# Kernel optimization log

Hardware: AMD Instinct MI355X
Metric: run time of the kernel (lower is better)

Reference implementation:

```python
import jax, jax.numpy as jnp
import numpy as np

IMAGE_SIZE = 288.0
LAMBDA_NOOBJ = 0.5
LAMBDA_COOR = 5.0
_ANCHOR_DIMS = np.array([[0.24, 0.24], [0.12, 0.12], [0.08, 0.08], [0.28, 0.28], [0.15, 0.15]], np.float32)
ANCHORS = jnp.concatenate([jnp.full((5, 2), 0.5, jnp.float32), jnp.asarray(_ANCHOR_DIMS)], axis=1)  # [cx,cy,w,h]


def _corners(box):
    # matches torch _format_bbox column order used in _get_iou: (x1, x2, y1, y2)
    cx, cy, w, h = box[..., 0], box[..., 1], box[..., 2], box[..., 3]
    return cx - w / 2, cx + w / 2, cy - h / 2, cy + h / 2


def _iou(b1, b2):
    x1a, x2a, y1a, y2a = _corners(b1)
    x1b, x2b, y1b, y2b = _corners(b2)
    iw = jnp.minimum(x2a, x2b) - jnp.maximum(x1a, x1b) + 1.0
    ih = jnp.minimum(y2a, y2b) - jnp.maximum(y1a, y1b) + 1.0
    inter = iw * ih
    a1 = (x2a - x1a + 1.0) * (y2a - y1a + 1.0)
    a2 = (x2b - x1b + 1.0) * (y2b - y1b + 1.0)
    return inter / (a1 + a2 - inter + 1e-16)


def setup_inputs() -> dict:
    key = jax.random.key(0)
    k1, k2, k3, k4 = jax.random.split(key, 4)
    B, G, A, T = 32, 36, 5, 8
    return {
        "bbox_prediction": jax.random.normal(k1, (B, G, G, A, 5), jnp.float32),
        "landmarks_prediction": jax.random.normal(k2, (B, G, G, A, 68, 2), jnp.float32),
        "bbox_target": jax.random.uniform(k3, (B, T, 4), jnp.float32),
        "landmarks_target": jax.random.uniform(k4, (B, T, 68, 2), jnp.float32),
    }


def _forward(bbox_prediction, landmarks_prediction, bbox_target, landmarks_target):
    B, G, _, A, _ = bbox_prediction.shape
    T = bbox_target.shape[1]
    N = B * G * G * A

    valid = bbox_target.sum(-1) != 0  # (B,T)
    gx = bbox_target[..., 0] * G
    gy = bbox_target[..., 1] * G
    gi = jnp.floor(gx).astype(jnp.int32)  # int(gt_x)
    gj = jnp.floor(gy).astype(jnp.int32)
    fx = gx - gi
    fy = gy - gj
    gt_anchor_box = jnp.stack([fx, fy, bbox_target[..., 2], bbox_target[..., 3]], -1)  # (B,T,4)

    # vectorized anchor assignment (replaces per-target python loop)
    anchor_iou = _iou(gt_anchor_box[:, :, None, :], ANCHORS[None, None, :, :])  # (B,T,A)
    best_a = jnp.argmax(anchor_iou, -1).astype(jnp.int32)
    log_box = jnp.log1p(gt_anchor_box)  # (B,T,4) -- torch stores log1p form

    lin = ((jnp.arange(B)[:, None] * G + gj) * G + gi) * A + best_a  # (B,T) flat (b,j,i,a)
    lin = jnp.where(valid, lin, N)  # invalid targets -> dump slot N

    obj = jnp.zeros(N + 1, jnp.float32).at[lin.ravel()].set(1.0)[:N].reshape(B, G, G, A)
    noobj = 1.0 - obj

    t_ids = jnp.broadcast_to(jnp.arange(T, dtype=jnp.int32), (B, T))
    seg_last = jax.ops.segment_max(t_ids.ravel(), lin.ravel(), num_segments=N + 1)
    winner = (seg_last[lin] == t_ids) & valid
    lin_w = jnp.where(winner, lin, N).ravel()

    gt_boxes = jnp.zeros((N + 1, 4), jnp.float32).at[lin_w].set(log_box.reshape(-1, 4))[:N].reshape(B, G, G, A, 4)
    gt_lm = jnp.zeros((N + 1, 136), jnp.float32).at[lin_w].set(landmarks_target.reshape(B * T, 136))[:N].reshape(B, G, G, A, 136)

    nobj = jnp.maximum(obj.sum(), 1.0)

    # NME over object cells (masked-mean expressed as weighted sum -> static shapes)
    diff = landmarks_prediction.reshape(B, G, G, A, 136) - gt_lm
    dist = jnp.sqrt(jnp.sum(diff * diff, -1))  # (B,G,G,A)
    wh = gt_boxes[..., 2] * gt_boxes[..., 3]  # note: log1p(w)*log1p(h), as in torch
    norm = jnp.sqrt(jnp.where(obj > 0, wh, 1.0)) * IMAGE_SIZE * 68.0 * nobj
    nme = jnp.sum(obj * dist / norm)

    # localization: SmoothL1 (beta=1), mean over masked elements
    d = bbox_prediction[..., :4] - gt_boxes
    ad = jnp.abs(d)
    sl1 = jnp.where(ad < 1.0, 0.5 * d * d, ad - 0.5)
    loc_loss = LAMBDA_COOR * jnp.sum(obj[..., None] * sl1) / (nobj * 4.0)

    # confidence: MSE on noobj (target 0) + MSE on obj (target 1)
    conf_pred = bbox_prediction[..., 4]
    n_noobj = jnp.maximum(noobj.sum(), 1.0)
    conf_loss = LAMBDA_NOOBJ * jnp.sum(noobj * conf_pred ** 2) / n_noobj + jnp.sum(obj * (conf_pred - 1.0) ** 2) / nobj

    # best predicted bbox per target (IoU of log1p gt box vs raw cell predictions, as in torch)
    cell_pred = bbox_prediction[jnp.arange(B)[:, None], gj, gi]  # (B,T,A,5)
    pred_iou = _iou(log_box[:, :, None, :], cell_pred[..., :4])  # (B,T,A)
    best_p = jnp.argmax(pred_iou, -1)
    best = jnp.take_along_axis(cell_pred, best_p[..., None, None], axis=2)[:, :, 0]  # (B,T,5)
    x1, x2, y1, y2 = _corners(best[..., :4])
    best_pred = jnp.where(valid[..., None], jnp.stack([x1, x2, y1, y2, best[..., 4]], -1), 0.0)

    return nme, loc_loss, conf_loss, best_pred


def reference(bbox_prediction, landmarks_prediction, bbox_target, landmarks_target):
    return _forward(bbox_prediction, landmarks_prediction, bbox_target, landmarks_target)
```

## Files before the change

kernel.cpp:

```cpp
#include <hip/hip_runtime.h>
#include <math.h>

#define Gc 36
#define Ac 5
#define Bc 32
#define Tc 8
#define NCELLS (Bc*Gc*Gc*Ac)
#define NFLOATS (NCELLS*5)
#define NF4 (NFLOATS/4)
#define NT 256
#define CONF_BLOCKS 128


__device__ __forceinline__ void target_meta(const float* __restrict__ bbox_tgt,
                                            int tid, bool& valid, int& gi, int& gj,
                                            float& fx, float& fy, float& w, float& h,
                                            int& best_a) {
    const int b = tid >> 3, t = tid & 7;
    const float* tg = bbox_tgt + (size_t)(b * Tc + t) * 4;
    float x = tg[0], y = tg[1];
    w = tg[2]; h = tg[3];
    valid = ((x + y + w + h) != 0.0f);
    float gx = x * (float)Gc, gy = y * (float)Gc;
    gi = (int)floorf(gx); gj = (int)floorf(gy);
    fx = gx - floorf(gx); fy = gy - floorf(gy);

    float x1a = fx - w * 0.5f, x2a = fx + w * 0.5f;
    float y1a = fy - h * 0.5f, y2a = fy + h * 0.5f;
    float a1 = (x2a - x1a + 1.0f) * (y2a - y1a + 1.0f);
    const float adim[Ac] = {0.24f, 0.12f, 0.08f, 0.28f, 0.15f};
    best_a = 0;
    float best_iou = -1e30f;
    for (int a = 0; a < Ac; ++a) {
        float x1b = 0.5f - adim[a] * 0.5f, x2b = 0.5f + adim[a] * 0.5f;
        float iw = fminf(x2a, x2b) - fmaxf(x1a, x1b) + 1.0f;
        float ih = fminf(y2a, x2b) - fmaxf(y1a, x1b) + 1.0f;
        float inter = iw * ih;
        float a2 = (x2b - x1b + 1.0f) * (x2b - x1b + 1.0f);
        float iou = inter / (a1 + a2 - inter + 1e-16f);
        if (iou > best_iou) { best_iou = iou; best_a = a; }
    }
}

__global__ __launch_bounds__(NT) void k1_conf_meta(
        const float* __restrict__ bbox_pred,
        const float* __restrict__ bbox_tgt,
        float* __restrict__ ws_f, int* __restrict__ ws_i) {
    if (blockIdx.x < CONF_BLOCKS) {
        __shared__ float red[NT];
        const float4* p4 = (const float4*)bbox_pred;
        float acc = 0.0f;
        for (int j = blockIdx.x * NT + threadIdx.x; j < NF4;
             j += CONF_BLOCKS * NT) {
            float4 f = p4[j];
            int r = (4 * j) % 5;
            float v = (r == 4) ? f.x : (r == 3) ? f.y : (r == 2) ? f.z
                    : (r == 1) ? f.w : 0.0f;
            acc += v * v;
        }
        red[threadIdx.x] = acc;
        __syncthreads();
        for (int s = NT / 2; s > 0; s >>= 1) {
            if (threadIdx.x < s) red[threadIdx.x] += red[threadIdx.x + s];
            __syncthreads();
        }
        if (threadIdx.x == 0) ws_f[blockIdx.x] = red[0];
    } else {
        __shared__ int s_lin[NT];
        const int tid = threadIdx.x;
        const int b = tid >> 3, t = tid & 7;
        bool valid; int gi, gj, best_a; float fx, fy, w, h;
        target_meta(bbox_tgt, tid, valid, gi, gj, fx, fy, w, h, best_a);
        int lin = valid ? (((b * Gc + gj) * Gc + gi) * Ac + best_a) : NCELLS;
        s_lin[tid] = lin;
        __syncthreads();
        bool winner = valid;
        if (valid) {
            for (int t2 = t + 1; t2 < Tc; ++t2)
                if (s_lin[(b << 3) + t2] == lin) { winner = false; break; }
        }
        ws_i[256 + tid] = lin;
        ws_i[512 + tid] = winner ? 1 : 0;
    }
}

__global__ __launch_bounds__(64) void k2_lmdist(
        const float* __restrict__ lm_pred,
        const float* __restrict__ lm_tgt,
        const int* __restrict__ ws_i,
        float* __restrict__ ws_f) {
    const int tgt = blockIdx.x;
    const int lane = threadIdx.x;
    int winner = ws_i[512 + tgt];
    int lin = ws_i[256 + tgt];
    float acc = 0.0f;
    if (winner && lane < 34) {
        const float4* lp = (const float4*)(lm_pred + (size_t)lin * 136);
        const float4* lt = (const float4*)(lm_tgt + (size_t)tgt * 136);
        float4 a = lp[lane], b = lt[lane];
        float dx = a.x - b.x, dy = a.y - b.y, dz = a.z - b.z, dw = a.w - b.w;
        acc = dx * dx + dy * dy + dz * dz + dw * dw;
    }
    for (int off = 32; off > 0; off >>= 1)
        acc += __shfl_down(acc, off, 64);
    if (lane == 0) ws_f[1024 + tgt] = winner ? sqrtf(acc) : 0.0f;
}

__device__ __forceinline__ float block_sum(float v, float* red, int tid) {
    red[tid] = v;
    __syncthreads();
    for (int s = NT / 2; s > 0; s >>= 1) {
        if (tid < s) red[tid] += red[tid + s];
        __syncthreads();
    }
    float r = red[0];
    __syncthreads();
    return r;
}

__global__ __launch_bounds__(NT) void k3_final(
        const float* __restrict__ bbox_pred,
        const float* __restrict__ bbox_tgt,
        const float* __restrict__ ws_f,
        const int* __restrict__ ws_i,
        float* __restrict__ out) {
    const int tid = threadIdx.x;
    const int b = tid >> 3, t = tid & 7;
    __shared__ float s_red[NT];
    __shared__ int s_cnt[NT];

    bool valid; int gi, gj, best_a; float fx, fy, w, h;
    target_meta(bbox_tgt, tid, valid, gi, gj, fx, fy, w, h, best_a);
    int lin = ws_i[256 + tid];
    int winner = ws_i[512 + tid];
    float dist = ws_f[1024 + tid];

    float l0 = log1pf(fx), l1 = log1pf(fy), l2 = log1pf(w), l3 = log1pf(h);

    float c_nme = 0.0f, c_sl1 = 0.0f, c_cobj = 0.0f, c_csq = 0.0f;
    if (winner) {
        const float* bp = bbox_pred + (size_t)lin * 5;
        float conf = bp[4];
        c_cobj = (conf - 1.0f) * (conf - 1.0f);
        c_csq = conf * conf;
        float lb[4] = {l0, l1, l2, l3};
        for (int k = 0; k < 4; ++k) {
            float d = bp[k] - lb[k];
            float ad = fabsf(d);
            c_sl1 += (ad < 1.0f) ? 0.5f * d * d : (ad - 0.5f);
        }
        c_nme = dist / (sqrtf(l2 * l3) * 288.0f * 68.0f);
    }

    s_cnt[tid] = winner;
    __syncthreads();
    for (int s = NT / 2; s > 0; s >>= 1) {
        if (tid < s) s_cnt[tid] += s_cnt[tid + s];
        __syncthreads();
    }
    int cnt = s_cnt[0];
    __syncthreads();
    float nobj = fmaxf((float)cnt, 1.0f);
    float n_noobj = fmaxf((float)(NCELLS - cnt), 1.0f);

    float sum_nme  = block_sum(c_nme, s_red, tid);
    float sum_sl1  = block_sum(c_sl1, s_red, tid);
    float sum_cobj = block_sum(c_cobj, s_red, tid);
    float sum_csq  = block_sum(c_csq, s_red, tid);
    float s_total  = block_sum(tid < CONF_BLOCKS ? ws_f[tid] : 0.0f, s_red, tid);

    if (tid == 0) {
        out[0] = sum_nme / nobj;
        out[1] = 5.0f * sum_sl1 / (nobj * 4.0f);
        out[2] = 0.5f * (s_total - sum_csq) / n_noobj + sum_cobj / nobj;
    }

    const float* cp = bbox_pred + (size_t)((b * Gc + gj) * Gc + gi) * Ac * 5;
    float x1g = l0 - l2 * 0.5f, x2g = l0 + l2 * 0.5f;
    float y1g = l1 - l3 * 0.5f, y2g = l1 + l3 * 0.5f;
    float ag = (x2g - x1g + 1.0f) * (y2g - y1g + 1.0f);
    int bp_idx = 0;
    float bp_iou = -1e30f;
    for (int a = 0; a < Ac; ++a) {
        float cx = cp[a * 5 + 0], cy = cp[a * 5 + 1];
        float pw = cp[a * 5 + 2], ph = cp[a * 5 + 3];
        float x1p = cx - pw * 0.5f, x2p = cx + pw * 0.5f;
        float y1p = cy - ph * 0.5f, y2p = cy + ph * 0.5f;
        float iw = fminf(x2g, x2p) - fmaxf(x1g, x1p) + 1.0f;
        float ih = fminf(y2g, y2p) - fmaxf(y1g, y1p) + 1.0f;
        float inter = iw * ih;
        float ap = (x2p - x1p + 1.0f) * (y2p - y1p + 1.0f);
        float iou = inter / (ag + ap - inter + 1e-16f);
        if (iou > bp_iou) { bp_iou = iou; bp_idx = a; }
    }
    float bx = cp[bp_idx * 5 + 0], by = cp[bp_idx * 5 + 1];
    float bw = cp[bp_idx * 5 + 2], bh = cp[bp_idx * 5 + 3];
    float bconf = cp[bp_idx * 5 + 4];
    float* op = out + 3 + (size_t)tid * 5;
    if (valid) {
        op[0] = bx - bw * 0.5f; op[1] = bx + bw * 0.5f;
        op[2] = by - bh * 0.5f; op[3] = by + bh * 0.5f; op[4] = bconf;
    } else {
        op[0] = 0.0f; op[1] = 0.0f; op[2] = 0.0f; op[3] = 0.0f; op[4] = 0.0f;
    }
}

extern "C" void kernel_launch(void* const* d_in, const int* in_sizes, int n_in,
                              void* d_out, int out_size, void* d_ws, size_t ws_size,
                              hipStream_t stream) {
    const float* bbox_pred = (const float*)d_in[0];
    const float* lm_pred   = (const float*)d_in[1];
    const float* bbox_tgt  = (const float*)d_in[2];
    const float* lm_tgt    = (const float*)d_in[3];
    float* out = (float*)d_out;
    float* ws_f = (float*)d_ws;
    int* ws_i = (int*)d_ws;

    k1_conf_meta<<<CONF_BLOCKS + 1, NT, 0, stream>>>(bbox_pred, bbox_tgt, ws_f, ws_i);
    k2_lmdist<<<256, 64, 0, stream>>>(lm_pred, lm_tgt, ws_i, ws_f);
    k3_final<<<1, NT, 0, stream>>>(bbox_pred, bbox_tgt, ws_f, ws_i, out);
}
```

Baseline: 160.3 us.

## Fuse landmark distance kernel into conf reduction kernel, one block per target

Merges the target-metadata block and the landmark-distance kernel into the confidence-sum kernel. Each of 256 extra blocks recomputes the metadata for its batch's 8 targets, dedups them in shared memory, and computes one target's landmark L2 distance. This removes one kernel launch and the dependency between them. In exchange the metadata is computed redundantly across blocks, and each 256-thread block uses only 64 threads.

```diff
diff --git a/kernel.cpp b/kernel.cpp
--- a/kernel.cpp
+++ b/kernel.cpp
@@ -13,11 +13,10 @@
 
 
 __device__ __forceinline__ void target_meta(const float* __restrict__ bbox_tgt,
-                                            int tid, bool& valid, int& gi, int& gj,
+                                            int tgt, bool& valid, int& gi, int& gj,
                                             float& fx, float& fy, float& w, float& h,
                                             int& best_a) {
-    const int b = tid >> 3, t = tid & 7;
-    const float* tg = bbox_tgt + (size_t)(b * Tc + t) * 4;
+    const float* tg = bbox_tgt + (size_t)tgt * 4;
     float x = tg[0], y = tg[1];
     w = tg[2]; h = tg[3];
     valid = ((x + y + w + h) != 0.0f);
@@ -42,9 +41,11 @@
     }
 }
 
-__global__ __launch_bounds__(NT) void k1_conf_meta(
+__global__ __launch_bounds__(NT) void k12_conf_lm(
         const float* __restrict__ bbox_pred,
+        const float* __restrict__ lm_pred,
         const float* __restrict__ bbox_tgt,
+        const float* __restrict__ lm_tgt,
         float* __restrict__ ws_f, int* __restrict__ ws_i) {
     if (blockIdx.x < CONF_BLOCKS) {
         __shared__ float red[NT];
@@ -66,44 +67,45 @@
         }
         if (threadIdx.x == 0) ws_f[blockIdx.x] = red[0];
     } else {
-        __shared__ int s_lin[NT];
+        const int tgt = blockIdx.x - CONF_BLOCKS;
+        const int b = tgt >> 3, t = tgt & 7;
         const int tid = threadIdx.x;
-        const int b = tid >> 3, t = tid & 7;
-        bool valid; int gi, gj, best_a; float fx, fy, w, h;
-        target_meta(bbox_tgt, tid, valid, gi, gj, fx, fy, w, h, best_a);
-        int lin = valid ? (((b * Gc + gj) * Gc + gi) * Ac + best_a) : NCELLS;
-        s_lin[tid] = lin;
-        __syncthreads();
-        bool winner = valid;
-        if (valid) {
-            for (int t2 = t + 1; t2 < Tc; ++t2)
-                if (s_lin[(b << 3) + t2] == lin) { winner = false; break; }
-        }
-        ws_i[256 + tid] = lin;
-        ws_i[512 + tid] = winner ? 1 : 0;
-    }
-}
-
-__global__ __launch_bounds__(64) void k2_lmdist(
-        const float* __restrict__ lm_pred,
-        const float* __restrict__ lm_tgt,
-        const int* __restrict__ ws_i,
-        float* __restrict__ ws_f) {
-    const int tgt = blockIdx.x;
-    const int lane = threadIdx.x;
-    int winner = ws_i[512 + tgt];
-    int lin = ws_i[256 + tgt];
-    float acc = 0.0f;
-    if (winner && lane < 34) {
-        const float4* lp = (const float4*)(lm_pred + (size_t)lin * 136);
-        const float4* lt = (const float4*)(lm_tgt + (size_t)tgt * 136);
-        float4 a = lp[lane], b = lt[lane];
-        float dx = a.x - b.x, dy = a.y - b.y, dz = a.z - b.z, dw = a.w - b.w;
-        acc = dx * dx + dy * dy + dz * dz + dw * dw;
-    }
-    for (int off = 32; off > 0; off >>= 1)
-        acc += __shfl_down(acc, off, 64);
-    if (lane == 0) ws_f[1024 + tgt] = winner ? sqrtf(acc) : 0.0f;
+        __shared__ int s_lin8[8];
+
+        if (tid < 8) {
+            bool v; int gi, gj, ba; float fx, fy, w, h;
+            target_meta(bbox_tgt, (b << 3) + tid, v, gi, gj, fx, fy, w, h, ba);
+            s_lin8[tid] = v ? (((b * Gc + gj) * Gc + gi) * Ac + ba) : NCELLS;
+        }
+        __syncthreads();
+
+        if (tid < 64) {
+            int lin = s_lin8[t];
+            bool valid = (lin != NCELLS);
+            bool winner = valid;
+            if (valid)
+                for (int t2 = t + 1; t2 < Tc; ++t2)
+                    if (s_lin8[t2] == lin) { winner = false; break; }
+
+            float acc = 0.0f;
+            if (winner && tid < 34) {
+                const float4* lp = (const float4*)(lm_pred + (size_t)lin * 136);
+                const float4* lt = (const float4*)(lm_tgt + (size_t)tgt * 136);
+                float4 a = lp[tid], c = lt[tid];
+                float dx = a.x - c.x, dy = a.y - c.y;
+                float dz = a.z - c.z, dw = a.w - c.w;
+                acc = dx * dx + dy * dy + dz * dz + dw * dw;
+            }
+            for (int off = 32; off > 0; off >>= 1)
+                acc += __shfl_down(acc, off, 64);
+
+            if (tid == 0) {
+                ws_i[256 + tgt] = lin;
+                ws_i[512 + tgt] = winner ? 1 : 0;
+                ws_f[1024 + tgt] = winner ? sqrtf(acc) : 0.0f;
+            }
+        }
+    }
 }
 
 __device__ __forceinline__ float block_sum(float v, float* red, int tid) {
@@ -125,7 +127,7 @@
         const int* __restrict__ ws_i,
         float* __restrict__ out) {
     const int tid = threadIdx.x;
-    const int b = tid >> 3, t = tid & 7;
+    const int b = tid >> 3;
     __shared__ float s_red[NT];
     __shared__ int s_cnt[NT];
 
@@ -216,7 +218,8 @@
     float* ws_f = (float*)d_ws;
     int* ws_i = (int*)d_ws;
 
-    k1_conf_meta<<<CONF_BLOCKS + 1, NT, 0, stream>>>(bbox_pred, bbox_tgt, ws_f, ws_i);
-    k2_lmdist<<<256, 64, 0, stream>>>(lm_pred, lm_tgt, ws_i, ws_f);
+    k12_conf_lm<<<CONF_BLOCKS + 256, NT, 0, stream>>>(bbox_pred, lm_pred,
+                                                      bbox_tgt, lm_tgt,
+                                                      ws_f, ws_i);
     k3_final<<<1, NT, 0, stream>>>(bbox_pred, bbox_tgt, ws_f, ws_i, out);
 }
```

Result: no change. 157.5 us (-1.8%).
